# Optimization experiments

Measured on AMD Instinct MI355X. Metric: run time of the kernel, lower is better.

## Reference

```python
import jax, jax.numpy as jnp
import numpy as np
from jax import lax

# Reconstruction of MVC (manifold/log-domain voxel conv):
#   log_forward : v = Conv3d(Log_M(x), w) in the log domain, base point M = per-voxel
#                 geometric mean over input channels (Log_M(x) = log x - log M on R+).
#   exp_forward : out = Exp_M(v) = M * exp(v).
# The custom autograd (grad_x + grad_M) corresponds to input gradients flowing through
# both the log-domain conv and the base point M.

B, CIN, COUT, K = 2, 16, 16, 3
D = H = W = 96


def setup_inputs() -> dict:
    key = jax.random.key(0)
    k1, k2 = jax.random.split(key)
    # strictly positive voxel values (fODF coefficients) so log is well-defined
    x = jax.random.uniform(k1, (B, CIN, D, H, W), dtype=jnp.float32,
                           minval=0.05, maxval=1.0)
    weights = jax.random.uniform(k2, (COUT, K, K, K, CIN), dtype=jnp.float32)
    return {"x": x, "weights": weights}


def reference(x, weights):
    logx = jnp.log(x)                                   # [B, Cin, D, H, W]
    logM = jnp.mean(logx, axis=1, keepdims=True)        # per-voxel base point, [B,1,D,H,W]
    # log_forward: 3D conv of tangent vectors (log x - log M)
    w = jnp.transpose(weights, (0, 4, 1, 2, 3))         # [Cout, Cin, K, K, K] (OIDHW)
    conv = lax.conv_general_dilated(
        logx, w, window_strides=(1, 1, 1), padding='SAME',
        dimension_numbers=('NCDHW', 'OIDHW', 'NCDHW'))  # [B, Cout, D, H, W]
    wsum = jnp.sum(weights, axis=(1, 2, 3, 4))          # [Cout], accounts for -logM term
    out_log = conv - wsum[None, :, None, None, None] * logM
    # exp_forward: Exp_M(v) = M * exp(v) = exp(logM + v)
    return jnp.exp(logM + out_log)
```

## Files before the change

### kernel.cpp

```cpp
#include <hip/hip_runtime.h>


#define VOXn (96 * 96 * 96)
#define SLY  6
#define SLX  98
#define ROWS (SLX * 16)
#define SS   (SLY * ROWS)
#define TYv  4
#define ZC   6

typedef __attribute__((ext_vector_type(8))) short short8;
typedef __attribute__((ext_vector_type(4))) float f32x4;

__device__ __forceinline__ unsigned short f2bf_rne(float f) {
    unsigned u = __float_as_uint(f);
    u += 0x7fff + ((u >> 16) & 1);
    return (unsigned short)(u >> 16);
}
__device__ __forceinline__ float bf2f(short s) {
    return __uint_as_float(((unsigned)(unsigned short)s) << 16);
}

__global__ void mvc_reorg(const float* __restrict__ w,
                          short* __restrict__ w3,
                          float* __restrict__ wadj) {
    int i = blockIdx.x * 256 + threadIdx.x;
    if (i < 16 * 448) {
        int n = i / 448, k = i % 448;
        int p = k >> 5, q = (k >> 3) & 3, j = k & 7;
        int qhi = q >> 1, ci = (q & 1) * 8 + j;
        int tap;
        bool valid = true;
        if (p < 9)        tap = (p / 3) * 9 + (p % 3) * 3 + qhi;
        else if (p < 12)  tap = (p - 9) * 9 + qhi * 3 + 2;
        else if (p == 12) tap = qhi * 9 + 8;
        else { tap = 26; valid = (qhi == 0); }
        float v = valid ? w[n * 432 + tap * 16 + ci] : 0.0f;
        w3[i] = (short)f2bf_rne(v);
    }
    if (i < 16) {
        const float* pw = w + i * 432;
        float s = 0.0f;
        for (int t = 0; t < 432; ++t) s += pw[t];
        wadj[i] = 1.0f - s;
    }
}

__global__ void __launch_bounds__(256, 2)
mvc_main(const float* __restrict__ x,
         const short* __restrict__ w3,
         const float* __restrict__ wadj,
         float* __restrict__ out) {
    __shared__ __align__(16) short tile[3 * SS];
    __shared__ float logMt[TYv * 96];

    const int tid  = threadIdx.x;
    const int lane = tid & 63;
    const int wv   = tid >> 6;
    const int mn   = lane & 15;
    const int q    = lane >> 4;
    const int qlo  = q & 1;
    const int qhi  = q >> 1;

    int id  = blockIdx.x;
    int xcd = id & 7, g = id >> 3;
    int yt  = xcd * 3 + g % 3;
    int rr  = g / 3;
    int zch = rr & 15, b = rr >> 4;
    const int y0 = yt * TYv;
    const int z0 = zch * ZC;

    const float* xb = x + (size_t)b * 16 * VOXn;
    float* ob = out + (size_t)b * 16 * VOXn;

    short8 bfr[14];
    #pragma unroll
    for (int p = 0; p < 14; ++p)
        bfr[p] = *(const short8*)(w3 + mn * 448 + p * 32 + q * 8);
    const float4 wv4 = *(const float4*)(wadj + 4 * q);
    const float wa[4] = {wv4.x, wv4.y, wv4.z, wv4.w};

    if (tid < 288) {
        int d = tid & 7, vv = tid >> 3;
        int bu = vv / 12, rv = vv % 12;
        int row = rv >> 1, side = rv & 1;
        ((unsigned*)tile)[bu * (SS / 2) + (row * SLX + side * 97) * 8 + d] = 0u;
    }

    float2 h[5][4];

    auto load_plane = [&](int zp) {
        bool zin = (unsigned)zp < 96u;
        #pragma unroll
        for (int it = 0; it < 5; ++it) {
            if (it == 4 && tid >= 128) break;
            int slot = tid + it * 256;
            int cq = slot & 3;
            int t  = slot >> 2;
            int xp = t % 48;
            int y  = t / 48;
            int gy = y0 + y - 1;
            bool inb = zin && ((unsigned)gy < 96u);
            const float* p0 = xb + (size_t)(4 * cq) * VOXn
                            + ((zp * 96 + gy) * 96 + 2 * xp);
            h[it][0] = inb ? *(const float2*)(p0)            : make_float2(1.f, 1.f);
            h[it][1] = inb ? *(const float2*)(p0 + VOXn)     : make_float2(1.f, 1.f);
            h[it][2] = inb ? *(const float2*)(p0 + 2 * VOXn) : make_float2(1.f, 1.f);
            h[it][3] = inb ? *(const float2*)(p0 + 3 * VOXn) : make_float2(1.f, 1.f);
        }
    };
    auto write_plane = [&](int zp) {
        short* sb = tile + ((zp + 3) % 3) * SS;
        #pragma unroll
        for (int it = 0; it < 5; ++it) {
            if (it == 4 && tid >= 128) break;
            int slot = tid + it * 256;
            int cq = slot & 3;
            int t  = slot >> 2;
            int xp = t % 48;
            int y  = t / 48;
            unsigned a0 = f2bf_rne(__logf(h[it][0].x)), a1 = f2bf_rne(__logf(h[it][1].x));
            unsigned a2 = f2bf_rne(__logf(h[it][2].x)), a3 = f2bf_rne(__logf(h[it][3].x));
            unsigned c0 = f2bf_rne(__logf(h[it][0].y)), c1 = f2bf_rne(__logf(h[it][1].y));
            unsigned c2 = f2bf_rne(__logf(h[it][2].y)), c3 = f2bf_rne(__logf(h[it][3].y));
            unsigned* dst = (unsigned*)(sb + (y * SLX + 1 + 2 * xp) * 16 + 4 * cq);
            *(uint2*)(dst)     = make_uint2(a0 | (a1 << 16), a2 | (a3 << 16));
            *(uint2*)(dst + 8) = make_uint2(c0 | (c1 << 16), c2 | (c3 << 16));
        }
    };
    auto do_logM = [&](int z) {
        const short* cb = tile + (z % 3) * SS;
        #pragma unroll
        for (int it = 0; it < 2; ++it) {
            if (it == 1 && tid >= 128) break;
            int v = tid + it * 256;
            int xx = v % 96, yy = v / 96;
            const short* p = cb + ((yy + 1) * SLX + (xx + 1)) * 16;
            short8 h0 = *(const short8*)p;
            short8 h1 = *(const short8*)(p + 8);
            float s = 0.f;
            #pragma unroll
            for (int c = 0; c < 8; ++c) s += bf2f(h0[c]) + bf2f(h1[c]);
            logMt[v] = s * 0.0625f;
        }
    };

    load_plane(z0 - 1); write_plane(z0 - 1);
    load_plane(z0);     write_plane(z0);
    load_plane(z0 + 1); write_plane(z0 + 1);
    __syncthreads();

    for (int zi = 0; zi < ZC; ++zi) {
        const int z = z0 + zi;
        const bool st = (zi < ZC - 1);
        if (st) load_plane(z + 2);
        do_logM(z);
        __syncthreads();

        const int B0 = ((z + 2) % 3) * SS;
        const int B1 = (z % 3) * SS;
        const int B2 = ((z + 1) % 3) * SS;
        const int Lb = mn * 16 + qlo * 8 + wv * ROWS + qhi * 16;

        #pragma unroll
        for (int j = 0; j < 6; ++j) {
            const short* vA0 = tile + (Lb + j * 256 + B0);
            const short* vA1 = tile + (Lb + j * 256 + B1);
            const short* vA2 = tile + (Lb + j * 256 + B2);
            const short* vB0 = vA0 + 32 + qhi * 1552;
            const short* vB1 = vA1 + 32 + qhi * 1552;
            const short* vB2 = vA2 + 32 + qhi * 1552;
            const short* vD  = vB2 + (3136 - qhi * 1584);
            const short* vC  = vD - B2 + (qhi ? B1 : B0);

            f32x4 acc = {0.f, 0.f, 0.f, 0.f};
            acc = __builtin_amdgcn_mfma_f32_16x16x32_bf16(bfr[0],  *(const short8*)(vA0),        acc, 0, 0, 0);
            acc = __builtin_amdgcn_mfma_f32_16x16x32_bf16(bfr[1],  *(const short8*)(vA0 + 1568), acc, 0, 0, 0);
            acc = __builtin_amdgcn_mfma_f32_16x16x32_bf16(bfr[2],  *(const short8*)(vA0 + 3136), acc, 0, 0, 0);
            acc = __builtin_amdgcn_mfma_f32_16x16x32_bf16(bfr[3],  *(const short8*)(vA1),        acc, 0, 0, 0);
            acc = __builtin_amdgcn_mfma_f32_16x16x32_bf16(bfr[4],  *(const short8*)(vA1 + 1568), acc, 0, 0, 0);
            acc = __builtin_amdgcn_mfma_f32_16x16x32_bf16(bfr[5],  *(const short8*)(vA1 + 3136), acc, 0, 0, 0);
            acc = __builtin_amdgcn_mfma_f32_16x16x32_bf16(bfr[6],  *(const short8*)(vA2),        acc, 0, 0, 0);
            acc = __builtin_amdgcn_mfma_f32_16x16x32_bf16(bfr[7],  *(const short8*)(vA2 + 1568), acc, 0, 0, 0);
            acc = __builtin_amdgcn_mfma_f32_16x16x32_bf16(bfr[8],  *(const short8*)(vA2 + 3136), acc, 0, 0, 0);
            acc = __builtin_amdgcn_mfma_f32_16x16x32_bf16(bfr[9],  *(const short8*)(vB0),        acc, 0, 0, 0);
            acc = __builtin_amdgcn_mfma_f32_16x16x32_bf16(bfr[10], *(const short8*)(vB1),        acc, 0, 0, 0);
            acc = __builtin_amdgcn_mfma_f32_16x16x32_bf16(bfr[11], *(const short8*)(vB2),        acc, 0, 0, 0);
            acc = __builtin_amdgcn_mfma_f32_16x16x32_bf16(bfr[12], *(const short8*)(vC),         acc, 0, 0, 0);
            acc = __builtin_amdgcn_mfma_f32_16x16x32_bf16(bfr[13], *(const short8*)(vD),         acc, 0, 0, 0);

            float lm = logMt[wv * 96 + j * 16 + mn];
            float* op = ob + (size_t)(4 * q) * VOXn
                      + (((size_t)z * 96 + (y0 + wv)) * 96 + j * 16 + mn);
            #pragma unroll
            for (int r = 0; r < 4; ++r) {
                float e = fminf(fmaf(wa[r], lm, acc[r]), 88.0f);
                op[(size_t)r * VOXn] = __expf(e);
            }
        }
        __syncthreads();
        if (st) write_plane(z + 2);
    }
}

extern "C" void kernel_launch(void* const* d_in, const int* in_sizes, int n_in,
                              void* d_out, int out_size, void* d_ws, size_t ws_size,
                              hipStream_t stream) {
    const float* x = (const float*)d_in[0];
    const float* w = (const float*)d_in[1];
    float* out  = (float*)d_out;
    short* w3   = (short*)d_ws;
    float* wadj = (float*)((char*)d_ws + 16 * 448 * 2);

    hipLaunchKernelGGL(mvc_reorg, dim3(28), dim3(256), 0, stream, w, w3, wadj);
    hipLaunchKernelGGL(mvc_main, dim3(768), dim3(256), 0, stream, x, w3, wadj, out);
}
```

Before: 289.5 us.

## Split log precompute into separate kernel and stream bf16 planes via global_load_lds

Adds a pre-pass kernel that takes the log of x once and stores it as channel-interleaved bf16 in workspace. The conv kernel then streams z-planes straight into a 4-slot LDS ring with global_load_lds, with no per-thread log/convert or register staging. It also computes logM with an extra MFMA against a constant 1/16 vector instead of a separate LDS reduction pass and barrier. Tiles are retuned to 2 y-rows by 12 z-planes, and the old fused kernel stays as a fallback when workspace is too small. In exchange the bf16 log tensor makes an extra round trip through global memory.

```diff
diff --git a/kernel.cpp b/kernel.cpp
--- a/kernel.cpp
+++ b/kernel.cpp
@@ -1,13 +1,15 @@
 #include <hip/hip_runtime.h>
 
 
-#define VOXn (96 * 96 * 96)
-#define SLY  6
+#define VOX  884736
 #define SLX  98
 #define ROWS (SLX * 16)
-#define SS   (SLY * ROWS)
-#define TYv  4
-#define ZC   6
+#define SROWS 4
+#define SSs  (SROWS * ROWS)
+#define SSb  (SSs * 2)
+#define NSL  4
+#define TY   2
+#define ZC   12
 
 typedef __attribute__((ext_vector_type(8))) short short8;
 typedef __attribute__((ext_vector_type(4))) float f32x4;
@@ -46,13 +48,30 @@
     }
 }
 
-__global__ void __launch_bounds__(256, 2)
-mvc_main(const float* __restrict__ x,
+__global__ void __launch_bounds__(256)
+mvc_log(const float* __restrict__ x, short* __restrict__ lx) {
+    const int id = blockIdx.x;
+    const int b = id / 3456;
+    const size_t v = (size_t)(id - b * 3456) * 256 + threadIdx.x;
+    const float* xb = x + (size_t)b * 16 * VOX + v;
+    unsigned rbuf[8];
+    #pragma unroll
+    for (int c = 0; c < 8; ++c) {
+        unsigned lo = f2bf_rne(__logf(xb[(size_t)(2 * c) * VOX]));
+        unsigned hi = f2bf_rne(__logf(xb[(size_t)(2 * c + 1) * VOX]));
+        rbuf[c] = lo | (hi << 16);
+    }
+    unsigned* dst = (unsigned*)(lx + ((size_t)b * VOX + v) * 16);
+    *(uint4*)dst       = make_uint4(rbuf[0], rbuf[1], rbuf[2], rbuf[3]);
+    *(uint4*)(dst + 4) = make_uint4(rbuf[4], rbuf[5], rbuf[6], rbuf[7]);
+}
+
+__global__ void __launch_bounds__(256, 3)
+mvc_conv(const short* __restrict__ lx,
          const short* __restrict__ w3,
          const float* __restrict__ wadj,
          float* __restrict__ out) {
-    __shared__ __align__(16) short tile[3 * SS];
-    __shared__ float logMt[TYv * 96];
+    __shared__ __align__(16) short tile[NSL * SSs + 512];
 
     const int tid  = threadIdx.x;
     const int lane = tid & 63;
@@ -64,14 +83,14 @@
 
     int id  = blockIdx.x;
     int xcd = id & 7, g = id >> 3;
-    int yt  = xcd * 3 + g % 3;
-    int rr  = g / 3;
-    int zch = rr & 15, b = rr >> 4;
-    const int y0 = yt * TYv;
+    int yt  = xcd * 6 + g % 6;
+    int rr  = g / 6;
+    int zch = rr % 8, b = rr / 8;
+    const int y0 = yt * TY;
     const int z0 = zch * ZC;
 
-    const float* xb = x + (size_t)b * 16 * VOXn;
-    float* ob = out + (size_t)b * 16 * VOXn;
+    const short* lxb = lx + (size_t)b * VOX * 16;
+    float* ob = out + (size_t)b * 16 * VOX;
 
     short8 bfr[14];
     #pragma unroll
@@ -79,91 +98,75 @@
         bfr[p] = *(const short8*)(w3 + mn * 448 + p * 32 + q * 8);
     const float4 wv4 = *(const float4*)(wadj + 4 * q);
     const float wa[4] = {wv4.x, wv4.y, wv4.z, wv4.w};
-
-    if (tid < 288) {
-        int d = tid & 7, vv = tid >> 3;
-        int bu = vv / 12, rv = vv % 12;
-        int row = rv >> 1, side = rv & 1;
-        ((unsigned*)tile)[bu * (SS / 2) + (row * SLX + side * 97) * 8 + d] = 0u;
-    }
-
-    float2 h[5][4];
-
-    auto load_plane = [&](int zp) {
-        bool zin = (unsigned)zp < 96u;
-        #pragma unroll
-        for (int it = 0; it < 5; ++it) {
-            if (it == 4 && tid >= 128) break;
-            int slot = tid + it * 256;
-            int cq = slot & 3;
-            int t  = slot >> 2;
-            int xp = t % 48;
-            int y  = t / 48;
-            int gy = y0 + y - 1;
-            bool inb = zin && ((unsigned)gy < 96u);
-            const float* p0 = xb + (size_t)(4 * cq) * VOXn
-                            + ((zp * 96 + gy) * 96 + 2 * xp);
-            h[it][0] = inb ? *(const float2*)(p0)            : make_float2(1.f, 1.f);
-            h[it][1] = inb ? *(const float2*)(p0 + VOXn)     : make_float2(1.f, 1.f);
-            h[it][2] = inb ? *(const float2*)(p0 + 2 * VOXn) : make_float2(1.f, 1.f);
-            h[it][3] = inb ? *(const float2*)(p0 + 3 * VOXn) : make_float2(1.f, 1.f);
+    const short oc = qhi ? (short)0x3D80 : (short)0;
+    const short8 aones = {oc, oc, oc, oc, oc, oc, oc, oc};
+
+    auto stage = [&](int zp) {
+        const int sl = zp & 3;
+        const int gy = y0 - 1 + wv;
+        const bool vr = (unsigned)gy < 96u;
+        const int gyc = vr ? gy : 0;
+        const short* gsrc = lxb + (size_t)(zp * 9216 + gyc * 96) * 16 + lane * 8;
+        short* lrow = tile + sl * SSs + (wv * SLX + 1) * 16;
+        short* ltr  = tile + NSL * SSs;
+        #pragma unroll
+        for (int k = 0; k < 3; ++k) {
+            short* dst = vr ? (lrow + k * 512) : ltr;
+            __builtin_amdgcn_global_load_lds(
+                (const __attribute__((address_space(1))) unsigned int*)(const void*)(gsrc + k * 512),
+                (__attribute__((address_space(3))) unsigned int*)(void*)dst,
+                16, 0, 0);
         }
     };
-    auto write_plane = [&](int zp) {
-        short* sb = tile + ((zp + 3) % 3) * SS;
-        #pragma unroll
-        for (int it = 0; it < 5; ++it) {
-            if (it == 4 && tid >= 128) break;
-            int slot = tid + it * 256;
-            int cq = slot & 3;
-            int t  = slot >> 2;
-            int xp = t % 48;
-            int y  = t / 48;
-            unsigned a0 = f2bf_rne(__logf(h[it][0].x)), a1 = f2bf_rne(__logf(h[it][1].x));
-            unsigned a2 = f2bf_rne(__logf(h[it][2].x)), a3 = f2bf_rne(__logf(h[it][3].x));
-            unsigned c0 = f2bf_rne(__logf(h[it][0].y)), c1 = f2bf_rne(__logf(h[it][1].y));
-            unsigned c2 = f2bf_rne(__logf(h[it][2].y)), c3 = f2bf_rne(__logf(h[it][3].y));
-            unsigned* dst = (unsigned*)(sb + (y * SLX + 1 + 2 * xp) * 16 + 4 * cq);
-            *(uint2*)(dst)     = make_uint2(a0 | (a1 << 16), a2 | (a3 << 16));
-            *(uint2*)(dst + 8) = make_uint2(c0 | (c1 << 16), c2 | (c3 << 16));
+    auto zero_slice = [&](int sl) {
+        #pragma unroll
+        for (int i = 0; i < 4; ++i) {
+            int c = tid + i * 256;
+            if (c < 784)
+                *(f32x4*)((char*)tile + sl * SSb + c * 16) = (f32x4){0.f, 0.f, 0.f, 0.f};
         }
     };
-    auto do_logM = [&](int z) {
-        const short* cb = tile + (z % 3) * SS;
-        #pragma unroll
-        for (int it = 0; it < 2; ++it) {
-            if (it == 1 && tid >= 128) break;
-            int v = tid + it * 256;
-            int xx = v % 96, yy = v / 96;
-            const short* p = cb + ((yy + 1) * SLX + (xx + 1)) * 16;
-            short8 h0 = *(const short8*)p;
-            short8 h1 = *(const short8*)(p + 8);
-            float s = 0.f;
-            #pragma unroll
-            for (int c = 0; c < 8; ++c) s += bf2f(h0[c]) + bf2f(h1[c]);
-            logMt[v] = s * 0.0625f;
-        }
-    };
-
-    load_plane(z0 - 1); write_plane(z0 - 1);
-    load_plane(z0);     write_plane(z0);
-    load_plane(z0 + 1); write_plane(z0 + 1);
-    __syncthreads();
-
+
+    if (tid < 64) {
+        int s = tid >> 4, rest = tid & 15;
+        int row = rest >> 2, side = (rest >> 1) & 1, half = tid & 1;
+        *(f32x4*)((char*)tile + s * SSb + (row * SLX + side * 97) * 32 + half * 16)
+            = (f32x4){0.f, 0.f, 0.f, 0.f};
+    }
+    if (yt == 0 || yt == 47) {
+        int row = (yt == 0) ? 0 : 3;
+        #pragma unroll
+        for (int s = 0; s < 4; ++s)
+            if (tid < 196)
+                *(f32x4*)((char*)tile + s * SSb + row * 3136 + tid * 16)
+                    = (f32x4){0.f, 0.f, 0.f, 0.f};
+    }
+    if (z0 == 0) zero_slice(3); else stage(z0 - 1);
+    stage(z0);
+    stage(z0 + 1);
+
+    #pragma unroll 1
     for (int zi = 0; zi < ZC; ++zi) {
         const int z = z0 + zi;
-        const bool st = (zi < ZC - 1);
-        if (st) load_plane(z + 2);
-        do_logM(z);
+        asm volatile("s_waitcnt vmcnt(0)" ::: "memory");
         __syncthreads();
-
-        const int B0 = ((z + 2) % 3) * SS;
-        const int B1 = (z % 3) * SS;
-        const int B2 = ((z + 1) % 3) * SS;
-        const int Lb = mn * 16 + qlo * 8 + wv * ROWS + qhi * 16;
-
-        #pragma unroll
-        for (int j = 0; j < 6; ++j) {
+        if (zi < ZC - 1) {
+            const int zp = z + 2;
+            if (zp < 96) stage(zp);
+            else         zero_slice(zp & 3);
+        }
+        __builtin_amdgcn_sched_barrier(0);
+
+        const int B0 = ((z + 3) & 3) * SSs;
+        const int B1 = (z & 3) * SSs;
+        const int B2 = ((z + 1) & 3) * SSs;
+        const int r  = wv >> 1;
+        const int xh = wv & 1;
+        const int Lb = mn * 16 + qlo * 8 + r * ROWS + qhi * 16;
+
+        #pragma unroll
+        for (int jj = 0; jj < 3; ++jj) {
+            const int j = xh * 3 + jj;
             const short* vA0 = tile + (Lb + j * 256 + B0);
             const short* vA1 = tile + (Lb + j * 256 + B1);
             const short* vA2 = tile + (Lb + j * 256 + B2);
@@ -189,13 +192,177 @@
             acc = __builtin_amdgcn_mfma_f32_16x16x32_bf16(bfr[12], *(const short8*)(vC),         acc, 0, 0, 0);
             acc = __builtin_amdgcn_mfma_f32_16x16x32_bf16(bfr[13], *(const short8*)(vD),         acc, 0, 0, 0);
 
+            f32x4 am = __builtin_amdgcn_mfma_f32_16x16x32_bf16(
+                aones, *(const short8*)(vA1 + 1568), (f32x4){0.f, 0.f, 0.f, 0.f}, 0, 0, 0);
+            const float lm = am[0];
+
+            float* op = ob + (size_t)(4 * q) * VOX
+                      + (((size_t)z * 96 + (y0 + r)) * 96 + j * 16 + mn);
+            #pragma unroll
+            for (int t = 0; t < 4; ++t) {
+                float e = fminf(fmaf(wa[t], lm, acc[t]), 88.0f);
+                op[(size_t)t * VOX] = __expf(e);
+            }
+        }
+    }
+}
+
+#define FSLY  6
+#define FROWS (SLX * 16)
+#define FSS   (FSLY * FROWS)
+#define FTY   4
+#define FZC   6
+
+__global__ void __launch_bounds__(256, 2)
+mvc_main(const float* __restrict__ x,
+         const short* __restrict__ w3,
+         const float* __restrict__ wadj,
+         float* __restrict__ out) {
+    __shared__ __align__(16) short tile[3 * FSS];
+    __shared__ float logMt[FTY * 96];
+
+    const int tid  = threadIdx.x;
+    const int lane = tid & 63;
+    const int wv   = tid >> 6;
+    const int mn   = lane & 15;
+    const int q    = lane >> 4;
+    const int qlo  = q & 1;
+    const int qhi  = q >> 1;
+
+    int id  = blockIdx.x;
+    int xcd = id & 7, g = id >> 3;
+    int yt  = xcd * 3 + g % 3;
+    int rr  = g / 3;
+    int zch = rr & 15, b = rr >> 4;
+    const int y0 = yt * FTY;
+    const int z0 = zch * FZC;
+
+    const float* xb = x + (size_t)b * 16 * VOX;
+    float* ob = out + (size_t)b * 16 * VOX;
+
+    short8 bfr[14];
+    #pragma unroll
+    for (int p = 0; p < 14; ++p)
+        bfr[p] = *(const short8*)(w3 + mn * 448 + p * 32 + q * 8);
+    const float4 wv4 = *(const float4*)(wadj + 4 * q);
+    const float wa[4] = {wv4.x, wv4.y, wv4.z, wv4.w};
+
+    if (tid < 288) {
+        int d = tid & 7, vv = tid >> 3;
+        int bu = vv / 12, rv = vv % 12;
+        int row = rv >> 1, side = rv & 1;
+        ((unsigned*)tile)[bu * (FSS / 2) + (row * SLX + side * 97) * 8 + d] = 0u;
+    }
+
+    float2 h[5][4];
+
+    auto load_plane = [&](int zp) {
+        bool zin = (unsigned)zp < 96u;
+        #pragma unroll
+        for (int it = 0; it < 5; ++it) {
+            if (it == 4 && tid >= 128) break;
+            int slot = tid + it * 256;
+            int cq = slot & 3;
+            int t  = slot >> 2;
+            int xp = t % 48;
+            int y  = t / 48;
+            int gy = y0 + y - 1;
+            bool inb = zin && ((unsigned)gy < 96u);
+            const float* p0 = xb + (size_t)(4 * cq) * VOX
+                            + ((zp * 96 + gy) * 96 + 2 * xp);
+            h[it][0] = inb ? *(const float2*)(p0)            : make_float2(1.f, 1.f);
+            h[it][1] = inb ? *(const float2*)(p0 + VOX)      : make_float2(1.f, 1.f);
+            h[it][2] = inb ? *(const float2*)(p0 + 2 * VOX)  : make_float2(1.f, 1.f);
+            h[it][3] = inb ? *(const float2*)(p0 + 3 * VOX)  : make_float2(1.f, 1.f);
+        }
+    };
+    auto write_plane = [&](int zp) {
+        short* sb = tile + ((zp + 3) % 3) * FSS;
+        #pragma unroll
+        for (int it = 0; it < 5; ++it) {
+            if (it == 4 && tid >= 128) break;
+            int slot = tid + it * 256;
+            int cq = slot & 3;
+            int t  = slot >> 2;
+            int xp = t % 48;
+            int y  = t / 48;
+            unsigned a0 = f2bf_rne(__logf(h[it][0].x)), a1 = f2bf_rne(__logf(h[it][1].x));
+            unsigned a2 = f2bf_rne(__logf(h[it][2].x)), a3 = f2bf_rne(__logf(h[it][3].x));
+            unsigned c0 = f2bf_rne(__logf(h[it][0].y)), c1 = f2bf_rne(__logf(h[it][1].y));
+            unsigned c2 = f2bf_rne(__logf(h[it][2].y)), c3 = f2bf_rne(__logf(h[it][3].y));
+            unsigned* dst = (unsigned*)(sb + (y * SLX + 1 + 2 * xp) * 16 + 4 * cq);
+            *(uint2*)(dst)     = make_uint2(a0 | (a1 << 16), a2 | (a3 << 16));
+            *(uint2*)(dst + 8) = make_uint2(c0 | (c1 << 16), c2 | (c3 << 16));
+        }
+    };
+    auto do_logM = [&](int z) {
+        const short* cb = tile + (z % 3) * FSS;
+        #pragma unroll
+        for (int it = 0; it < 2; ++it) {
+            if (it == 1 && tid >= 128) break;
+            int v = tid + it * 256;
+            int xx = v % 96, yy = v / 96;
+            const short* p = cb + ((yy + 1) * SLX + (xx + 1)) * 16;
+            short8 h0 = *(const short8*)p;
+            short8 h1 = *(const short8*)(p + 8);
+            float s = 0.f;
+            #pragma unroll
+            for (int c = 0; c < 8; ++c) s += bf2f(h0[c]) + bf2f(h1[c]);
+            logMt[v] = s * 0.0625f;
+        }
+    };
+
+    load_plane(z0 - 1); write_plane(z0 - 1);
+    load_plane(z0);     write_plane(z0);
+    load_plane(z0 + 1); write_plane(z0 + 1);
+    __syncthreads();
+
+    for (int zi = 0; zi < FZC; ++zi) {
+        const int z = z0 + zi;
+        const bool st = (zi < FZC - 1);
+        if (st) load_plane(z + 2);
+        do_logM(z);
+        __syncthreads();
+
+        const int B0 = ((z + 2) % 3) * FSS;
+        const int B1 = (z % 3) * FSS;
+        const int B2 = ((z + 1) % 3) * FSS;
+        const int Lb = mn * 16 + qlo * 8 + wv * FROWS + qhi * 16;
+
+        #pragma unroll
+        for (int j = 0; j < 6; ++j) {
+            const short* vA0 = tile + (Lb + j * 256 + B0);
+            const short* vA1 = tile + (Lb + j * 256 + B1);
+            const short* vA2 = tile + (Lb + j * 256 + B2);
+            const short* vB0 = vA0 + 32 + qhi * 1552;
+            const short* vB1 = vA1 + 32 + qhi * 1552;
+            const short* vB2 = vA2 + 32 + qhi * 1552;
+            const short* vD  = vB2 + (3136 - qhi * 1584);
+            const short* vC  = vD - B2 + (qhi ? B1 : B0);
+
+            f32x4 acc = {0.f, 0.f, 0.f, 0.f};
+            acc = __builtin_amdgcn_mfma_f32_16x16x32_bf16(bfr[0],  *(const short8*)(vA0),        acc, 0, 0, 0);
+            acc = __builtin_amdgcn_mfma_f32_16x16x32_bf16(bfr[1],  *(const short8*)(vA0 + 1568), acc, 0, 0, 0);
+            acc = __builtin_amdgcn_mfma_f32_16x16x32_bf16(bfr[2],  *(const short8*)(vA0 + 3136), acc, 0, 0, 0);
+            acc = __builtin_amdgcn_mfma_f32_16x16x32_bf16(bfr[3],  *(const short8*)(vA1),        acc, 0, 0, 0);
+            acc = __builtin_amdgcn_mfma_f32_16x16x32_bf16(bfr[4],  *(const short8*)(vA1 + 1568), acc, 0, 0, 0);
+            acc = __builtin_amdgcn_mfma_f32_16x16x32_bf16(bfr[5],  *(const short8*)(vA1 + 3136), acc, 0, 0, 0);
+            acc = __builtin_amdgcn_mfma_f32_16x16x32_bf16(bfr[6],  *(const short8*)(vA2),        acc, 0, 0, 0);
+            acc = __builtin_amdgcn_mfma_f32_16x16x32_bf16(bfr[7],  *(const short8*)(vA2 + 1568), acc, 0, 0, 0);
+            acc = __builtin_amdgcn_mfma_f32_16x16x32_bf16(bfr[8],  *(const short8*)(vA2 + 3136), acc, 0, 0, 0);
+            acc = __builtin_amdgcn_mfma_f32_16x16x32_bf16(bfr[9],  *(const short8*)(vB0),        acc, 0, 0, 0);
+            acc = __builtin_amdgcn_mfma_f32_16x16x32_bf16(bfr[10], *(const short8*)(vB1),        acc, 0, 0, 0);
+            acc = __builtin_amdgcn_mfma_f32_16x16x32_bf16(bfr[11], *(const short8*)(vB2),        acc, 0, 0, 0);
+            acc = __builtin_amdgcn_mfma_f32_16x16x32_bf16(bfr[12], *(const short8*)(vC),         acc, 0, 0, 0);
+            acc = __builtin_amdgcn_mfma_f32_16x16x32_bf16(bfr[13], *(const short8*)(vD),         acc, 0, 0, 0);
+
             float lm = logMt[wv * 96 + j * 16 + mn];
-            float* op = ob + (size_t)(4 * q) * VOXn
+            float* op = ob + (size_t)(4 * q) * VOX
                       + (((size_t)z * 96 + (y0 + wv)) * 96 + j * 16 + mn);
             #pragma unroll
-            for (int r = 0; r < 4; ++r) {
-                float e = fminf(fmaf(wa[r], lm, acc[r]), 88.0f);
-                op[(size_t)r * VOXn] = __expf(e);
+            for (int t = 0; t < 4; ++t) {
+                float e = fminf(fmaf(wa[t], lm, acc[t]), 88.0f);
+                op[(size_t)t * VOX] = __expf(e);
             }
         }
         __syncthreads();
@@ -210,8 +377,25 @@
     const float* w = (const float*)d_in[1];
     float* out  = (float*)d_out;
     short* w3   = (short*)d_ws;
-    float* wadj = (float*)((char*)d_ws + 16 * 448 * 2);
+    float* wadj = (float*)((char*)d_ws + 14336);
+    short* lgx  = (short*)((char*)d_ws + 16384);
+
+    const size_t lx_full = (size_t)2 * VOX * 16 * 2;
+    const size_t lx_half = (size_t)VOX * 16 * 2;
 
     hipLaunchKernelGGL(mvc_reorg, dim3(28), dim3(256), 0, stream, w, w3, wadj);
-    hipLaunchKernelGGL(mvc_main, dim3(768), dim3(256), 0, stream, x, w3, wadj, out);
-}
+
+    if (ws_size >= 16384 + lx_full) {
+        hipLaunchKernelGGL(mvc_log,  dim3(6912), dim3(256), 0, stream, x, lgx);
+        hipLaunchKernelGGL(mvc_conv, dim3(768),  dim3(256), 0, stream, lgx, w3, wadj, out);
+    } else if (ws_size >= 16384 + lx_half) {
+        for (int b = 0; b < 2; ++b) {
+            hipLaunchKernelGGL(mvc_log,  dim3(3456), dim3(256), 0, stream,
+                               x + (size_t)b * 16 * VOX, lgx);
+            hipLaunchKernelGGL(mvc_conv, dim3(384),  dim3(256), 0, stream,
+                               lgx, w3, wadj, out + (size_t)b * 16 * VOX);
+        }
+    } else {
+        hipLaunchKernelGGL(mvc_main, dim3(768), dim3(256), 0, stream, x, w3, wadj, out);
+    }
+}
```

Result: faster. 242.7 us (-16.2%).

## Retile to 2-row slabs with 4-buffer ring, MFMA-computed logM, single barrier

Applied to the files above, without the earlier changes.

Each block now covers 2 y-rows and 12 z-planes, with a 4-slot shared ring of z-planes, so one barrier per plane suffices after the write. The per-voxel mean log is computed with an extra MFMA against a constant ones-fragment instead of a separate LDS reduction pass, which removes the logMt buffer and a sync. Log and exp switch to base-2 hardware ops, with the clamp raised to 126. Occupancy is raised to 3 blocks per SM. The trade-off is larger z-halo overhead relative to the smaller y tile, and the risk of a ring-buffer race if the barrier placement is wrong.

```diff
diff --git a/kernel.cpp b/kernel.cpp
--- a/kernel.cpp
+++ b/kernel.cpp
@@ -1,13 +1,15 @@
 #include <hip/hip_runtime.h>
 
 
-#define VOXn (96 * 96 * 96)
-#define SLY  6
+#define VOX  884736
 #define SLX  98
 #define ROWS (SLX * 16)
-#define SS   (SLY * ROWS)
-#define TYv  4
-#define ZC   6
+#define SROWS 4
+#define SSs  (SROWS * ROWS)
+#define SSb  (SSs * 2)
+#define NSL  4
+#define TY   2
+#define ZC   12
 
 typedef __attribute__((ext_vector_type(8))) short short8;
 typedef __attribute__((ext_vector_type(4))) float f32x4;
@@ -16,9 +18,6 @@
     unsigned u = __float_as_uint(f);
     u += 0x7fff + ((u >> 16) & 1);
     return (unsigned short)(u >> 16);
-}
-__device__ __forceinline__ float bf2f(short s) {
-    return __uint_as_float(((unsigned)(unsigned short)s) << 16);
 }
 
 __global__ void mvc_reorg(const float* __restrict__ w,
@@ -46,13 +45,12 @@
     }
 }
 
-__global__ void __launch_bounds__(256, 2)
-mvc_main(const float* __restrict__ x,
-         const short* __restrict__ w3,
-         const float* __restrict__ wadj,
-         float* __restrict__ out) {
-    __shared__ __align__(16) short tile[3 * SS];
-    __shared__ float logMt[TYv * 96];
+__global__ void __launch_bounds__(256, 3)
+mvc_fused(const float* __restrict__ x,
+          const short* __restrict__ w3,
+          const float* __restrict__ wadj,
+          float* __restrict__ out) {
+    __shared__ __align__(16) short tile[NSL * SSs];
 
     const int tid  = threadIdx.x;
     const int lane = tid & 63;
@@ -64,14 +62,14 @@
 
     int id  = blockIdx.x;
     int xcd = id & 7, g = id >> 3;
-    int yt  = xcd * 3 + g % 3;
-    int rr  = g / 3;
-    int zch = rr & 15, b = rr >> 4;
-    const int y0 = yt * TYv;
+    int yt  = xcd * 6 + g % 6;
+    int rr  = g / 6;
+    int zch = rr % 8, b = rr / 8;
+    const int y0 = yt * TY;
     const int z0 = zch * ZC;
 
-    const float* xb = x + (size_t)b * 16 * VOXn;
-    float* ob = out + (size_t)b * 16 * VOXn;
+    const float* xb = x + (size_t)b * 16 * VOX;
+    float* ob = out + (size_t)b * 16 * VOX;
 
     short8 bfr[14];
     #pragma unroll
@@ -79,21 +77,14 @@
         bfr[p] = *(const short8*)(w3 + mn * 448 + p * 32 + q * 8);
     const float4 wv4 = *(const float4*)(wadj + 4 * q);
     const float wa[4] = {wv4.x, wv4.y, wv4.z, wv4.w};
-
-    if (tid < 288) {
-        int d = tid & 7, vv = tid >> 3;
-        int bu = vv / 12, rv = vv % 12;
-        int row = rv >> 1, side = rv & 1;
-        ((unsigned*)tile)[bu * (SS / 2) + (row * SLX + side * 97) * 8 + d] = 0u;
-    }
-
-    float2 h[5][4];
-
+    const short oc = qhi ? (short)0x3D80 : (short)0;
+    const short8 aones = {oc, oc, oc, oc, oc, oc, oc, oc};
+
+    float2 h[3][4];
     auto load_plane = [&](int zp) {
         bool zin = (unsigned)zp < 96u;
         #pragma unroll
-        for (int it = 0; it < 5; ++it) {
-            if (it == 4 && tid >= 128) break;
+        for (int it = 0; it < 3; ++it) {
             int slot = tid + it * 256;
             int cq = slot & 3;
             int t  = slot >> 2;
@@ -101,69 +92,63 @@
             int y  = t / 48;
             int gy = y0 + y - 1;
             bool inb = zin && ((unsigned)gy < 96u);
-            const float* p0 = xb + (size_t)(4 * cq) * VOXn
+            const float* p0 = xb + (size_t)(4 * cq) * VOX
                             + ((zp * 96 + gy) * 96 + 2 * xp);
             h[it][0] = inb ? *(const float2*)(p0)            : make_float2(1.f, 1.f);
-            h[it][1] = inb ? *(const float2*)(p0 + VOXn)     : make_float2(1.f, 1.f);
-            h[it][2] = inb ? *(const float2*)(p0 + 2 * VOXn) : make_float2(1.f, 1.f);
-            h[it][3] = inb ? *(const float2*)(p0 + 3 * VOXn) : make_float2(1.f, 1.f);
+            h[it][1] = inb ? *(const float2*)(p0 + VOX)      : make_float2(1.f, 1.f);
+            h[it][2] = inb ? *(const float2*)(p0 + 2 * VOX)  : make_float2(1.f, 1.f);
+            h[it][3] = inb ? *(const float2*)(p0 + 3 * VOX)  : make_float2(1.f, 1.f);
         }
     };
     auto write_plane = [&](int zp) {
-        short* sb = tile + ((zp + 3) % 3) * SS;
+        short* sb = tile + ((zp + 4) & 3) * SSs;
         #pragma unroll
-        for (int it = 0; it < 5; ++it) {
-            if (it == 4 && tid >= 128) break;
+        for (int it = 0; it < 3; ++it) {
             int slot = tid + it * 256;
             int cq = slot & 3;
             int t  = slot >> 2;
             int xp = t % 48;
             int y  = t / 48;
-            unsigned a0 = f2bf_rne(__logf(h[it][0].x)), a1 = f2bf_rne(__logf(h[it][1].x));
-            unsigned a2 = f2bf_rne(__logf(h[it][2].x)), a3 = f2bf_rne(__logf(h[it][3].x));
-            unsigned c0 = f2bf_rne(__logf(h[it][0].y)), c1 = f2bf_rne(__logf(h[it][1].y));
-            unsigned c2 = f2bf_rne(__logf(h[it][2].y)), c3 = f2bf_rne(__logf(h[it][3].y));
+            unsigned a0 = f2bf_rne(__log2f(h[it][0].x)), a1 = f2bf_rne(__log2f(h[it][1].x));
+            unsigned a2 = f2bf_rne(__log2f(h[it][2].x)), a3 = f2bf_rne(__log2f(h[it][3].x));
+            unsigned c0 = f2bf_rne(__log2f(h[it][0].y)), c1 = f2bf_rne(__log2f(h[it][1].y));
+            unsigned c2 = f2bf_rne(__log2f(h[it][2].y)), c3 = f2bf_rne(__log2f(h[it][3].y));
             unsigned* dst = (unsigned*)(sb + (y * SLX + 1 + 2 * xp) * 16 + 4 * cq);
             *(uint2*)(dst)     = make_uint2(a0 | (a1 << 16), a2 | (a3 << 16));
             *(uint2*)(dst + 8) = make_uint2(c0 | (c1 << 16), c2 | (c3 << 16));
         }
     };
-    auto do_logM = [&](int z) {
-        const short* cb = tile + (z % 3) * SS;
-        #pragma unroll
-        for (int it = 0; it < 2; ++it) {
-            if (it == 1 && tid >= 128) break;
-            int v = tid + it * 256;
-            int xx = v % 96, yy = v / 96;
-            const short* p = cb + ((yy + 1) * SLX + (xx + 1)) * 16;
-            short8 h0 = *(const short8*)p;
-            short8 h1 = *(const short8*)(p + 8);
-            float s = 0.f;
-            #pragma unroll
-            for (int c = 0; c < 8; ++c) s += bf2f(h0[c]) + bf2f(h1[c]);
-            logMt[v] = s * 0.0625f;
-        }
-    };
-
+
+    if (tid < 64) {
+        int rec = tid >> 1, half = tid & 1;
+        int s = rec >> 3, rest = rec & 7;
+        int row = rest >> 1, side = rest & 1;
+        *(f32x4*)((char*)tile + s * SSb + (row * SLX + side * 97) * 32 + half * 16)
+            = (f32x4){0.f, 0.f, 0.f, 0.f};
+    }
     load_plane(z0 - 1); write_plane(z0 - 1);
     load_plane(z0);     write_plane(z0);
     load_plane(z0 + 1); write_plane(z0 + 1);
     __syncthreads();
 
+    const int r  = wv >> 1;
+    const int xh = wv & 1;
+    const int Lb = mn * 16 + qlo * 8 + r * ROWS + qhi * 16;
+
+    #pragma unroll 1
     for (int zi = 0; zi < ZC; ++zi) {
         const int z = z0 + zi;
         const bool st = (zi < ZC - 1);
         if (st) load_plane(z + 2);
-        do_logM(z);
-        __syncthreads();
-
-        const int B0 = ((z + 2) % 3) * SS;
-        const int B1 = (z % 3) * SS;
-        const int B2 = ((z + 1) % 3) * SS;
-        const int Lb = mn * 16 + qlo * 8 + wv * ROWS + qhi * 16;
+        __builtin_amdgcn_sched_barrier(0);
+
+        const int B0 = ((z + 3) & 3) * SSs;
+        const int B1 = (z & 3) * SSs;
+        const int B2 = ((z + 1) & 3) * SSs;
 
         #pragma unroll
-        for (int j = 0; j < 6; ++j) {
+        for (int jj = 0; jj < 3; ++jj) {
+            const int j = xh * 3 + jj;
             const short* vA0 = tile + (Lb + j * 256 + B0);
             const short* vA1 = tile + (Lb + j * 256 + B1);
             const short* vA2 = tile + (Lb + j * 256 + B2);
@@ -173,12 +158,14 @@
             const short* vD  = vB2 + (3136 - qhi * 1584);
             const short* vC  = vD - B2 + (qhi ? B1 : B0);
 
+            short8 cf = *(const short8*)(vA1 + 1568);
+
             f32x4 acc = {0.f, 0.f, 0.f, 0.f};
             acc = __builtin_amdgcn_mfma_f32_16x16x32_bf16(bfr[0],  *(const short8*)(vA0),        acc, 0, 0, 0);
             acc = __builtin_amdgcn_mfma_f32_16x16x32_bf16(bfr[1],  *(const short8*)(vA0 + 1568), acc, 0, 0, 0);
             acc = __builtin_amdgcn_mfma_f32_16x16x32_bf16(bfr[2],  *(const short8*)(vA0 + 3136), acc, 0, 0, 0);
             acc = __builtin_amdgcn_mfma_f32_16x16x32_bf16(bfr[3],  *(const short8*)(vA1),        acc, 0, 0, 0);
-            acc = __builtin_amdgcn_mfma_f32_16x16x32_bf16(bfr[4],  *(const short8*)(vA1 + 1568), acc, 0, 0, 0);
+            acc = __builtin_amdgcn_mfma_f32_16x16x32_bf16(bfr[4],  cf,                           acc, 0, 0, 0);
             acc = __builtin_amdgcn_mfma_f32_16x16x32_bf16(bfr[5],  *(const short8*)(vA1 + 3136), acc, 0, 0, 0);
             acc = __builtin_amdgcn_mfma_f32_16x16x32_bf16(bfr[6],  *(const short8*)(vA2),        acc, 0, 0, 0);
             acc = __builtin_amdgcn_mfma_f32_16x16x32_bf16(bfr[7],  *(const short8*)(vA2 + 1568), acc, 0, 0, 0);
@@ -189,17 +176,25 @@
             acc = __builtin_amdgcn_mfma_f32_16x16x32_bf16(bfr[12], *(const short8*)(vC),         acc, 0, 0, 0);
             acc = __builtin_amdgcn_mfma_f32_16x16x32_bf16(bfr[13], *(const short8*)(vD),         acc, 0, 0, 0);
 
-            float lm = logMt[wv * 96 + j * 16 + mn];
-            float* op = ob + (size_t)(4 * q) * VOXn
-                      + (((size_t)z * 96 + (y0 + wv)) * 96 + j * 16 + mn);
+            f32x4 am = __builtin_amdgcn_mfma_f32_16x16x32_bf16(
+                aones, cf, (f32x4){0.f, 0.f, 0.f, 0.f}, 0, 0, 0);
+            const float lm = am[0];
+
+            float* op = ob + (size_t)(4 * q) * VOX
+                      + (((size_t)z * 96 + (y0 + r)) * 96 + j * 16 + mn);
             #pragma unroll
-            for (int r = 0; r < 4; ++r) {
-                float e = fminf(fmaf(wa[r], lm, acc[r]), 88.0f);
-                op[(size_t)r * VOXn] = __expf(e);
+            for (int t = 0; t < 4; ++t) {
+                float e = fminf(fmaf(wa[t], lm, acc[t]), 126.0f);
+                op[(size_t)t * VOX] = __builtin_amdgcn_exp2f(e);
             }
         }
-        __syncthreads();
-        if (st) write_plane(z + 2);
+
+        if (st) {
+            write_plane(z + 2);
+            asm volatile("s_waitcnt lgkmcnt(0)" ::: "memory");
+            __builtin_amdgcn_s_barrier();
+            __builtin_amdgcn_sched_barrier(0);
+        }
     }
 }
 
@@ -210,8 +205,8 @@
     const float* w = (const float*)d_in[1];
     float* out  = (float*)d_out;
     short* w3   = (short*)d_ws;
-    float* wadj = (float*)((char*)d_ws + 16 * 448 * 2);
-
-    hipLaunchKernelGGL(mvc_reorg, dim3(28), dim3(256), 0, stream, w, w3, wadj);
-    hipLaunchKernelGGL(mvc_main, dim3(768), dim3(256), 0, stream, x, w3, wadj, out);
-}
+    float* wadj = (float*)((char*)d_ws + 14336);
+
+    hipLaunchKernelGGL(mvc_reorg, dim3(28),  dim3(256), 0, stream, w, w3, wadj);
+    hipLaunchKernelGGL(mvc_fused, dim3(768), dim3(256), 0, stream, x, w3, wadj, out);
+}
```

Measured after the change: 237.5 us. -18.0%, faster.
